# Optimization experiments

Hardware: AMD Instinct MI355X
Metric: run time of the kernel (lower is better)

## Reference

```python
import jax, jax.numpy as jnp
import numpy as np

N, E, D, C = 50000, 800000, 128, 7
BN_EPS = 1e-5


def _sage_conv(x, src, dst, Wl, Wr, b):
    # mean-aggregate neighbor messages per destination, then linear + root linear
    msgs = x[src]  # [E, D] irregular gather
    summed = jax.ops.segment_sum(msgs, dst, num_segments=N)
    cnt = jax.ops.segment_sum(jnp.ones((src.shape[0],), x.dtype), dst, num_segments=N)
    agg = summed / jnp.maximum(cnt, 1.0)[:, None]
    return agg @ Wl.T + x @ Wr.T + b


def _bn_eval(x, g, be):
    # running_mean=0, running_var=1 (eval mode)
    return x * (g / jnp.sqrt(1.0 + BN_EPS)) + be


def setup_inputs() -> dict:
    key = jax.random.key(0)
    ks = jax.random.split(key, 20)
    w = lambda k, s: jax.random.normal(k, s, dtype=jnp.float32) * 0.05
    inp = {
        "x": jax.random.normal(ks[0], (N, D), dtype=jnp.float32),
        "edge_index": jax.random.randint(ks[1], (2, E), 0, N, dtype=jnp.int64),
        "Wl0": w(ks[2], (D, D)), "Wr0": w(ks[3], (D, D)), "b0": jnp.zeros((D,), jnp.float32),
        "Wl1": w(ks[4], (D, D)), "Wr1": w(ks[5], (D, D)), "b1": jnp.zeros((D,), jnp.float32),
        "Wl2": w(ks[6], (D, D)), "Wr2": w(ks[7], (D, D)), "b2": jnp.zeros((D,), jnp.float32),
        "g0": jnp.ones((D,), jnp.float32), "be0": jnp.zeros((D,), jnp.float32),
        "g1": jnp.ones((D,), jnp.float32), "be1": jnp.zeros((D,), jnp.float32),
        "dW1": w(ks[8], (D, D)), "db1": jnp.zeros((D,), jnp.float32),
        "dW2": w(ks[9], (C, D)), "db2": jnp.zeros((C,), jnp.float32),
        "dW3": w(ks[10], (D, D)), "db3": jnp.zeros((D,), jnp.float32),
    }
    return inp


def reference(x, edge_index, Wl0, Wr0, b0, Wl1, Wr1, b1, Wl2, Wr2, b2,
              g0, be0, g1, be1, dW1, db1, dW2, db2, dW3, db3):
    src, dst = edge_index[0], edge_index[1]
    h = _sage_conv(x, src, dst, Wl0, Wr0, b0)
    h = jax.nn.relu(_bn_eval(h, g0, be0))  # dropout is identity in eval
    h = _sage_conv(h, src, dst, Wl1, Wr1, b1)
    h = jax.nn.relu(_bn_eval(h, g1, be1))
    h = _sage_conv(h, src, dst, Wl2, Wr2, b2)
    recon_x1 = h @ dW1.T + db1
    recon_x2 = h @ dW2.T + db2
    recon_x3 = h @ dW3.T + db3
    return (recon_x1, recon_x2, recon_x3)
```

## Files before the change

### kernel.cpp

```cpp
#include <hip/hip_runtime.h>
#include <hip/hip_fp16.h>

static constexpr float kBnEps = 1e-5f;
static constexpr int MAXB = 1024;

typedef __attribute__((ext_vector_type(8))) _Float16 f16x8;
typedef __attribute__((ext_vector_type(4))) float f32x4;

__device__ __forceinline__ int detect64(const int* __restrict__ eb) {
    int l = threadIdx.x & 63;
    int v = eb[2 * l + 1];
    unsigned long long m = __ballot(v == 0);
    return (m == ~0ull) ? 1 : 0;
}

__device__ __forceinline__ int edge_src(const int* eb, int is64, int E, int e) {
    return is64 ? eb[2 * e] : eb[e];
}
__device__ __forceinline__ int edge_dst(const int* eb, int is64, int E, int e) {
    return is64 ? eb[2 * E + 2 * e] : eb[E + e];
}

__global__ __launch_bounds__(256) void prep_k(
    const int* __restrict__ eb, int* __restrict__ gcnt, int E, int nbuck,
    const float* __restrict__ x, __half* __restrict__ x_h, int total8,
    const float* __restrict__ Wl0, const float* __restrict__ Wr0,
    const float* __restrict__ Wl1, const float* __restrict__ Wr1,
    const float* __restrict__ Wl2, const float* __restrict__ Wr2,
    const float* __restrict__ dW1, const float* __restrict__ dW3,
    const float* __restrict__ dW2, __half* __restrict__ Wcat,
    __half* __restrict__ dWcat, int HC, int CX) {
    __shared__ int lh[MAXB];
    int b = blockIdx.x;
    int tid = threadIdx.x;
    if (b < HC) {
        for (int i = tid; i < nbuck; i += 256) lh[i] = 0;
        __syncthreads();
        int is64 = detect64(eb);
        int base = b * 4096;
#pragma unroll
        for (int i = 0; i < 16; ++i) {
            int e = base + i * 256 + tid;
            if (e < E) {
                int d = edge_dst(eb, is64, E, e);
                atomicAdd(&lh[d >> 7], 1);
            }
        }
        __syncthreads();
        for (int i = tid; i < nbuck; i += 256) {
            int c = lh[i];
            if (c) atomicAdd(&gcnt[i], c);
        }
    } else if (b < HC + CX) {
        int i = (b - HC) * 256 + tid;
        if (i < total8) {
            float4 v0 = ((const float4*)x)[2 * i];
            float4 v1 = ((const float4*)x)[2 * i + 1];
            __half2 h0 = __floats2half2_rn(v0.x, v0.y);
            __half2 h1 = __floats2half2_rn(v0.z, v0.w);
            __half2 h2 = __floats2half2_rn(v1.x, v1.y);
            __half2 h3 = __floats2half2_rn(v1.z, v1.w);
            uint4 o;
            o.x = *(uint*)&h0; o.y = *(uint*)&h1; o.z = *(uint*)&h2; o.w = *(uint*)&h3;
            ((uint4*)x_h)[i] = o;
        }
    } else {
        int idx = (b - HC - CX) * 256 + tid;
        if (idx < 3 * 32768) {
            int l = idx >> 15;
            int rem = idx & 32767;
            int nn = rem >> 8;
            int k = rem & 255;
            const float* Wl = (l == 0) ? Wl0 : (l == 1) ? Wl1 : Wl2;
            const float* Wr = (l == 0) ? Wr0 : (l == 1) ? Wr1 : Wr2;
            float v = (k < 128) ? Wl[nn * 128 + k] : Wr[nn * 128 + (k - 128)];
            Wcat[idx] = __float2half_rn(v);
        } else if (idx < 3 * 32768 + 3 * 16384) {
            int j = idx - 3 * 32768;
            int blk = j >> 14;
            int r = (j & 16383) >> 7;
            int c = j & 127;
            float v;
            if (blk == 0) v = dW1[r * 128 + c];
            else if (blk == 1) v = dW3[r * 128 + c];
            else v = (r < 7) ? dW2[r * 128 + c] : 0.f;
            dWcat[j] = __float2half_rn(v);
        }
    }
}

__global__ __launch_bounds__(512) void scanB_k(const int* __restrict__ gcnt,
                                               int* __restrict__ gbase,
                                               int* __restrict__ gcur,
                                               int* __restrict__ offs, int E,
                                               int n, int nbuck) {
    __shared__ int s[512];
    int tid = threadIdx.x;
    int v = (tid < nbuck) ? gcnt[tid] : 0;
    s[tid] = v;
    __syncthreads();
    for (int d = 1; d < 512; d <<= 1) {
        int t = (tid >= d) ? s[tid - d] : 0;
        __syncthreads();
        s[tid] += t;
        __syncthreads();
    }
    if (tid < nbuck) {
        gbase[tid] = s[tid] - v;
        gcur[tid] = s[tid] - v;
    }
    if (tid == 0) {
        gbase[nbuck] = E;
        offs[n] = E;
    }
}

__global__ __launch_bounds__(256) void binC_k(const int* __restrict__ eb,
                                              int* __restrict__ gcur,
                                              unsigned* __restrict__ bins, int E,
                                              int nbuck) {
    __shared__ int lh[MAXB];
    __shared__ int lcur[MAXB];
    for (int i = threadIdx.x; i < nbuck; i += 256) lh[i] = 0;
    __syncthreads();
    int is64 = detect64(eb);
    int base = blockIdx.x * 4096;
    int ds[16], ss[16];
#pragma unroll
    for (int i = 0; i < 16; ++i) {
        int e = base + i * 256 + threadIdx.x;
        ds[i] = -1;
        if (e < E) {
            ds[i] = edge_dst(eb, is64, E, e);
            ss[i] = edge_src(eb, is64, E, e);
            atomicAdd(&lh[ds[i] >> 7], 1);
        }
    }
    __syncthreads();
    for (int b = threadIdx.x; b < nbuck; b += 256) {
        int c = lh[b];
        lcur[b] = c ? atomicAdd(&gcur[b], c) : 0;
    }
    __syncthreads();
#pragma unroll
    for (int i = 0; i < 16; ++i) {
        if (ds[i] >= 0) {
            int bkt = ds[i] >> 7;
            int p = atomicAdd(&lcur[bkt], 1);
            bins[p] = ((unsigned)ss[i] << 7) | (unsigned)(ds[i] & 127);
        }
    }
}

__global__ __launch_bounds__(256) void csrD_k(const unsigned* __restrict__ bins,
                                              const int* __restrict__ gbase,
                                              int* __restrict__ offs,
                                              int* __restrict__ csr, int n) {
    int b = blockIdx.x;
    __shared__ int hist[128];
    __shared__ int s[128];
    __shared__ int cur[128];
    int tid = threadIdx.x;
    if (tid < 128) hist[tid] = 0;
    __syncthreads();
    int base = gbase[b], endb = gbase[b + 1], m = endb - base;
    for (int i = tid; i < m; i += 256) atomicAdd(&hist[bins[base + i] & 127u], 1);
    __syncthreads();
    int v = 0;
    if (tid < 128) {
        v = hist[tid];
        s[tid] = v;
    }
    __syncthreads();
    for (int d = 1; d < 128; d <<= 1) {
        int t = (tid >= d && tid < 128) ? s[tid - d] : 0;
        __syncthreads();
        if (tid < 128) s[tid] += t;
        __syncthreads();
    }
    if (tid < 128) {
        int excl = s[tid] - v;
        int dst = b * 128 + tid;
        if (dst < n) offs[dst] = base + excl;
        cur[tid] = base + excl;
    }
    __syncthreads();
    for (int i = tid; i < m; i += 256) {
        unsigned u = bins[base + i];
        int p = atomicAdd(&cur[u & 127u], 1);
        csr[p] = (int)(u >> 7);
    }
}

__global__ void agg_k(const __half* __restrict__ Xh, const int* __restrict__ offs,
                      const int* __restrict__ csr, __half* __restrict__ aggh, int n) {
    int gt = blockIdx.x * blockDim.x + threadIdx.x;
    int wid = gt >> 6;
    int lane = threadIdx.x & 63;
    if (wid >= n) return;
    int beg = offs[wid], end = offs[wid + 1];
    int len = end - beg;
    const uint* Xp = (const uint*)Xh;
    float a0 = 0.f, a1 = 0.f;
    for (int j0 = 0; j0 < len; j0 += 8) {
        int idx[8];
        float w[8];
#pragma unroll
        for (int t = 0; t < 8; ++t) {
            int jj = j0 + t;
            bool ok = jj < len;
            idx[t] = csr[beg + (ok ? jj : 0)];
            w[t] = ok ? 1.f : 0.f;
        }
        uint v[8];
#pragma unroll
        for (int t = 0; t < 8; ++t)
            v[t] = Xp[(size_t)idx[t] * 64 + lane];
#pragma unroll
        for (int t = 0; t < 8; ++t) {
            __half2 h = *(__half2*)&v[t];
            a0 += w[t] * __low2float(h);
            a1 += w[t] * __high2float(h);
        }
    }
    float inv = 1.0f / fmaxf((float)len, 1.0f);
    __half2 o = __floats2half2_rn(a0 * inv, a1 * inv);
    ((uint*)aggh)[(size_t)wid * 64 + lane] = *(uint*)&o;
}

template <int KTOT, bool TWO_SRC, bool BN_RELU, bool OUT16, bool HEADS>
__global__ __launch_bounds__(256) void mgemm_k(
    const __half* __restrict__ A0, const __half* __restrict__ A1,
    const __half* __restrict__ Bw, const float* __restrict__ bias,
    const float* __restrict__ g, const float* __restrict__ be,
    void* __restrict__ outv, const float* __restrict__ bias2,
    void* __restrict__ outv2, const float* __restrict__ bias3,
    void* __restrict__ outv3, int n) {
    constexpr int ROWB = KTOT * 2 + 16;
    __shared__ char sA[128 * ROWB];

    int ncol = 128, ostride = 128;
    if (HEADS) {
        int y = blockIdx.y;
        Bw += (size_t)y * 128 * KTOT;
        if (y == 1) { bias = bias2; outv = outv2; }
        if (y == 2) { bias = bias3; outv = outv3; ncol = 7; ostride = 7; }
    }

    const int tid = threadIdx.x;
    const int lane = tid & 63;
    const int wid = tid >> 6;
    const int wm = wid & 1;
    const int wn = wid >> 1;
    const int row0 = blockIdx.x * 128;

    constexpr int CPR = KTOT / 8;
#pragma unroll
    for (int i = 0; i < (128 * CPR) / 256; ++i) {
        int idx = tid + i * 256;
        int r = idx / CPR;
        int c = idx % CPR;
        int rg = row0 + r;
        float4 v = make_float4(0.f, 0.f, 0.f, 0.f);
        if (rg < n) {
            if (TWO_SRC)
                v = (c < 16) ? *(const float4*)(A0 + (size_t)rg * 128 + c * 8)
                             : *(const float4*)(A1 + (size_t)rg * 128 + (c - 16) * 8);
            else
                v = *(const float4*)(A0 + (size_t)rg * 128 + c * 8);
        }
        *(float4*)(&sA[r * ROWB + c * 16]) = v;
    }

    f32x4 acc[4][4];
#pragma unroll
    for (int mi = 0; mi < 4; ++mi)
#pragma unroll
        for (int ni = 0; ni < 4; ++ni) acc[mi][ni] = (f32x4){0.f, 0.f, 0.f, 0.f};

    __syncthreads();

    const int bcol = wn * 64;
    constexpr int KH = KTOT / 128;
#pragma unroll
    for (int kh = 0; kh < KH; ++kh) {
        f16x8 bfr[4][4];
#pragma unroll
        for (int ni = 0; ni < 4; ++ni)
#pragma unroll
            for (int kt = 0; kt < 4; ++kt) {
                int col = bcol + ni * 16 + (lane & 15);
                int ko = kh * 128 + kt * 32 + (lane >> 4) * 8;
                bfr[ni][kt] = *(const f16x8*)(Bw + (size_t)col * KTOT + ko);
            }
#pragma unroll
        for (int mi = 0; mi < 4; ++mi) {
            int rl = wm * 64 + mi * 16 + (lane & 15);
            const char* base = &sA[rl * ROWB + kh * 256 + (lane >> 4) * 16];
            f16x8 afr[4];
#pragma unroll
            for (int kt = 0; kt < 4; ++kt) afr[kt] = *(const f16x8*)(base + kt * 64);
#pragma unroll
            for (int kt = 0; kt < 4; ++kt)
#pragma unroll
                for (int ni = 0; ni < 4; ++ni)
                    acc[mi][ni] = __builtin_amdgcn_mfma_f32_16x16x32_f16(
                        afr[kt], bfr[ni][kt], acc[mi][ni], 0, 0, 0);
        }
    }

#pragma unroll
    for (int ni = 0; ni < 4; ++ni) {
        int col = bcol + ni * 16 + (lane & 15);
        if (HEADS && col >= ncol) continue;
        float bv = bias[col];
        float gs = 0.f, bes = 0.f;
        if (BN_RELU) {
            gs = g[col] / sqrtf(1.0f + kBnEps);
            bes = be[col];
        }
#pragma unroll
        for (int mi = 0; mi < 4; ++mi) {
#pragma unroll
            for (int r = 0; r < 4; ++r) {
                int row = row0 + wm * 64 + mi * 16 + (lane >> 4) * 4 + r;
                if (row < n) {
                    float v = acc[mi][ni][r] + bv;
                    if (BN_RELU) v = fmaxf(v * gs + bes, 0.f);
                    if (OUT16)
                        ((__half*)outv)[(size_t)row * 128 + col] = __float2half_rn(v);
                    else
                        ((float*)outv)[(size_t)row * ostride + col] = v;
                }
            }
        }
    }
}

extern "C" void kernel_launch(void* const* d_in, const int* in_sizes, int n_in,
                              void* d_out, int out_size, void* d_ws, size_t ws_size,
                              hipStream_t stream) {
    const float* x   = (const float*)d_in[0];
    const int*   eb  = (const int*)d_in[1];
    const float* Wl0 = (const float*)d_in[2];
    const float* Wr0 = (const float*)d_in[3];
    const float* b0  = (const float*)d_in[4];
    const float* Wl1 = (const float*)d_in[5];
    const float* Wr1 = (const float*)d_in[6];
    const float* b1  = (const float*)d_in[7];
    const float* Wl2 = (const float*)d_in[8];
    const float* Wr2 = (const float*)d_in[9];
    const float* b2  = (const float*)d_in[10];
    const float* g0  = (const float*)d_in[11];
    const float* be0 = (const float*)d_in[12];
    const float* g1  = (const float*)d_in[13];
    const float* be1 = (const float*)d_in[14];
    const float* dW1 = (const float*)d_in[15];
    const float* db1 = (const float*)d_in[16];
    const float* dW2 = (const float*)d_in[17];
    const float* db2 = (const float*)d_in[18];
    const float* dW3 = (const float*)d_in[19];
    const float* db3 = (const float*)d_in[20];

    const int n = in_sizes[0] / 128;
    const int E = in_sizes[1] / 2;
    const int nbuck = (n + 127) >> 7;

    char* ws = (char*)d_ws;
    size_t off = 0;
    auto alloc = [&](size_t bytes) -> void* {
        void* p = ws + off;
        off = (off + bytes + 255) & ~(size_t)255;
        return p;
    };
    int*      gcnt  = (int*)alloc(MAXB * 4);
    int*      gbase = (int*)alloc((MAXB + 1) * 4);
    int*      gcur  = (int*)alloc(MAXB * 4);
    unsigned* bins  = (unsigned*)alloc((size_t)E * 4);
    int*      csr   = (int*)alloc((size_t)E * 4);
    int*      offs  = (int*)alloc((size_t)(n + 1) * 4);
    __half*   x_h   = (__half*)alloc((size_t)n * 128 * 2);
    __half*   agg_h = (__half*)alloc((size_t)n * 128 * 2);
    __half*   h0    = (__half*)alloc((size_t)n * 128 * 2);
    __half*   h1    = (__half*)alloc((size_t)n * 128 * 2);
    __half*   h2    = h0;
    __half*   Wcat  = (__half*)alloc(3 * 32768 * 2);
    __half*   dWcat = (__half*)alloc(3 * 16384 * 2);

    float* out0 = (float*)d_out;
    float* out1 = out0 + (size_t)n * 128;
    float* out2 = out1 + (size_t)n * 7;

    hipMemsetAsync(gcnt, 0, MAXB * 4, stream);

    const int ggrid = (n + 127) / 128;
    const int agg_grid = (n * 64 + 255) / 256;
    const int HC = (E + 4095) / 4096;
    const int CX = (n * 16 + 255) / 256;
    const int CW = (147456 + 255) / 256;

    prep_k<<<HC + CX + CW, 256, 0, stream>>>(eb, gcnt, E, nbuck, x, x_h, n * 16,
                                             Wl0, Wr0, Wl1, Wr1, Wl2, Wr2, dW1,
                                             dW3, dW2, Wcat, dWcat, HC, CX);
    scanB_k<<<1, 512, 0, stream>>>(gcnt, gbase, gcur, offs, E, n, nbuck);
    binC_k<<<HC, 256, 0, stream>>>(eb, gcur, bins, E, nbuck);
    csrD_k<<<nbuck, 256, 0, stream>>>(bins, gbase, offs, csr, n);

    agg_k<<<agg_grid, 256, 0, stream>>>(x_h, offs, csr, agg_h, n);
    mgemm_k<256, true, true, true, false><<<ggrid, 256, 0, stream>>>(
        agg_h, x_h, Wcat, b0, g0, be0, h0, nullptr, nullptr, nullptr, nullptr, n);
    agg_k<<<agg_grid, 256, 0, stream>>>(h0, offs, csr, agg_h, n);
    mgemm_k<256, true, true, true, false><<<ggrid, 256, 0, stream>>>(
        agg_h, h0, Wcat + 32768, b1, g1, be1, h1, nullptr, nullptr, nullptr,
        nullptr, n);
    agg_k<<<agg_grid, 256, 0, stream>>>(h1, offs, csr, agg_h, n);
    mgemm_k<256, true, false, true, false><<<ggrid, 256, 0, stream>>>(
        agg_h, h1, Wcat + 65536, b2, nullptr, nullptr, h2, nullptr, nullptr,
        nullptr, nullptr, n);
    mgemm_k<128, false, false, false, true><<<dim3(ggrid, 3), 256, 0, stream>>>(
        h2, nullptr, dWcat, db1, nullptr, nullptr, out0, db3, out2, db2,
        out1, n);
}
```

Before: 239.7 us.

## Split neighbor aggregation into feature quarters with 4-way edge parallelism per wave

The aggregation kernel now assigns each wave one node and one quarter of its feature row (16 uint = 32 halves). The four 16-lane subgroups of a wave gather different neighbor edges at once, and shuffle reductions combine their partial sums. Block indexing interleaves quarters so that the blocks working on one node group are scheduled close together, which is meant to improve L2 reuse of the gathered rows and raise memory-level parallelism for low-degree nodes (average degree is about 16). In exchange the kernel launches 4x as many waves, adds a cross-lane reduction, and each gathered row segment is only 64 bytes.

New measurement: 318.8 us. +33.0%, slower.

```diff
diff --git a/kernel.cpp b/kernel.cpp
--- a/kernel.cpp
+++ b/kernel.cpp
@@ -192,30 +192,40 @@
     }
 }
 
-__global__ void agg_k(const __half* __restrict__ Xh, const int* __restrict__ offs,
-                      const int* __restrict__ csr, __half* __restrict__ aggh, int n) {
-    int gt = blockIdx.x * blockDim.x + threadIdx.x;
-    int wid = gt >> 6;
+__global__ __launch_bounds__(256) void aggq_k(const __half* __restrict__ Xh,
+                                              const int* __restrict__ offs,
+                                              const int* __restrict__ csr,
+                                              __half* __restrict__ aggh, int n,
+                                              int ng) {
+    int bid = blockIdx.x;
+    int q = (bid & 7) >> 1;
+    int gi = (bid >> 3) * 2 + (bid & 1);
+    if (gi >= ng) return;
+    int wv = threadIdx.x >> 6;
     int lane = threadIdx.x & 63;
-    if (wid >= n) return;
-    int beg = offs[wid], end = offs[wid + 1];
-    int len = end - beg;
+    int sub = lane >> 4;
+    int lg = lane & 15;
+    int node = gi * 4 + wv;
+    if (node >= n) return;
+    int beg = offs[node];
+    int len = offs[node + 1] - beg;
+    int lm1 = (len > 0) ? len - 1 : 0;
     const uint* Xp = (const uint*)Xh;
     float a0 = 0.f, a1 = 0.f;
-    for (int j0 = 0; j0 < len; j0 += 8) {
+    for (int j0 = 0; j0 < len; j0 += 32) {
         int idx[8];
         float w[8];
 #pragma unroll
         for (int t = 0; t < 8; ++t) {
-            int jj = j0 + t;
+            int jj = j0 + t * 4 + sub;
             bool ok = jj < len;
-            idx[t] = csr[beg + (ok ? jj : 0)];
+            idx[t] = csr[beg + (ok ? jj : lm1)];
             w[t] = ok ? 1.f : 0.f;
         }
         uint v[8];
 #pragma unroll
         for (int t = 0; t < 8; ++t)
-            v[t] = Xp[(size_t)idx[t] * 64 + lane];
+            v[t] = Xp[(size_t)idx[t] * 64 + q * 16 + lg];
 #pragma unroll
         for (int t = 0; t < 8; ++t) {
             __half2 h = *(__half2*)&v[t];
@@ -223,9 +233,15 @@
             a1 += w[t] * __high2float(h);
         }
     }
-    float inv = 1.0f / fmaxf((float)len, 1.0f);
-    __half2 o = __floats2half2_rn(a0 * inv, a1 * inv);
-    ((uint*)aggh)[(size_t)wid * 64 + lane] = *(uint*)&o;
+    a0 += __shfl_xor(a0, 16, 64);
+    a0 += __shfl_xor(a0, 32, 64);
+    a1 += __shfl_xor(a1, 16, 64);
+    a1 += __shfl_xor(a1, 32, 64);
+    if (sub == 0) {
+        float inv = 1.0f / fmaxf((float)len, 1.0f);
+        __half2 o = __floats2half2_rn(a0 * inv, a1 * inv);
+        ((uint*)aggh)[(size_t)node * 64 + q * 16 + lg] = *(uint*)&o;
+    }
 }
 
 template <int KTOT, bool TWO_SRC, bool BN_RELU, bool OUT16, bool HEADS>
@@ -394,10 +410,11 @@
     hipMemsetAsync(gcnt, 0, MAXB * 4, stream);
 
     const int ggrid = (n + 127) / 128;
-    const int agg_grid = (n * 64 + 255) / 256;
     const int HC = (E + 4095) / 4096;
     const int CX = (n * 16 + 255) / 256;
     const int CW = (147456 + 255) / 256;
+    const int ng = (n + 3) / 4;
+    const int agg_grid = ((ng + 1) / 2) * 8;
 
     prep_k<<<HC + CX + CW, 256, 0, stream>>>(eb, gcnt, E, nbuck, x, x_h, n * 16,
                                              Wl0, Wr0, Wl1, Wr1, Wl2, Wr2, dW1,
@@ -406,14 +423,14 @@
     binC_k<<<HC, 256, 0, stream>>>(eb, gcur, bins, E, nbuck);
     csrD_k<<<nbuck, 256, 0, stream>>>(bins, gbase, offs, csr, n);
 
-    agg_k<<<agg_grid, 256, 0, stream>>>(x_h, offs, csr, agg_h, n);
+    aggq_k<<<agg_grid, 256, 0, stream>>>(x_h, offs, csr, agg_h, n, ng);
     mgemm_k<256, true, true, true, false><<<ggrid, 256, 0, stream>>>(
         agg_h, x_h, Wcat, b0, g0, be0, h0, nullptr, nullptr, nullptr, nullptr, n);
-    agg_k<<<agg_grid, 256, 0, stream>>>(h0, offs, csr, agg_h, n);
+    aggq_k<<<agg_grid, 256, 0, stream>>>(h0, offs, csr, agg_h, n, ng);
     mgemm_k<256, true, true, true, false><<<ggrid, 256, 0, stream>>>(
         agg_h, h0, Wcat + 32768, b1, g1, be1, h1, nullptr, nullptr, nullptr,
         nullptr, n);
-    agg_k<<<agg_grid, 256, 0, stream>>>(h1, offs, csr, agg_h, n);
+    aggq_k<<<agg_grid, 256, 0, stream>>>(h1, offs, csr, agg_h, n, ng);
     mgemm_k<256, true, false, true, false><<<ggrid, 256, 0, stream>>>(
         agg_h, h1, Wcat + 65536, b2, nullptr, nullptr, h2, nullptr, nullptr,
         nullptr, nullptr, n);
```
